# Kernel tuning notes

Measured on AMD Instinct MI355X. Metric: run time of the kernel, lower is better.

Reference implementation:

```python
import jax, jax.numpy as jnp
import numpy as np

B, V, M, H, L, T = 4, 2048, 8192, 64, 5, 4


def setup_inputs() -> dict:
    key = jax.random.key(0)
    ks = jax.random.split(key, 24)
    inp = {
        "input_llr": jax.random.normal(ks[0], (B, V), jnp.float32),
        "message_to_var_mapping": jax.random.randint(ks[1], (M,), 0, V, jnp.int32),
        "message_types": jax.random.randint(ks[2], (M,), 0, T, jnp.int32),
        "var_to_check_adjacency": jax.random.uniform(ks[3], (M, M), jnp.float32),
        "check_to_var_adjacency": jax.random.uniform(ks[4], (M, M), jnp.float32),
    }
    s = 0.05
    # input_embedding: Linear(1, H)
    inp["w_in"] = jax.random.normal(ks[5], (H,), jnp.float32) * s
    inp["b_in"] = jax.random.normal(ks[6], (H,), jnp.float32) * s
    # per-layer params, stacked over L iterations
    inp["type_emb"] = jax.random.normal(ks[7], (L, T, H), jnp.float32) * s
    inp["w1v"] = jax.random.normal(ks[8], (L, 2 * H, H), jnp.float32) * s
    inp["b1v"] = jax.random.normal(ks[9], (L, H), jnp.float32) * s
    inp["w2v"] = jax.random.normal(ks[10], (L, H, H), jnp.float32) * s
    inp["b2v"] = jax.random.normal(ks[11], (L, H), jnp.float32) * s
    inp["w1c"] = jax.random.normal(ks[12], (L, 2 * H, H), jnp.float32) * s
    inp["b1c"] = jax.random.normal(ks[13], (L, H), jnp.float32) * s
    inp["w2c"] = jax.random.normal(ks[14], (L, H, H), jnp.float32) * s
    inp["b2c"] = jax.random.normal(ks[15], (L, H), jnp.float32) * s
    # output_projection of the LAST gnn layer (the one used by decode_messages)
    inp["proj_w"] = jax.random.normal(ks[16], (H,), jnp.float32) * s
    inp["proj_b"] = jax.random.normal(ks[17], (), jnp.float32) * s
    return inp


def reference(input_llr, message_to_var_mapping, message_types,
              var_to_check_adjacency, check_to_var_adjacency,
              w_in, b_in, type_emb, w1v, b1v, w2v, b2v,
              w1c, b1c, w2c, b2c, proj_w, proj_b):
    Bv, Vn = input_llr.shape
    # gather message LLRs from variable nodes: (B, M)
    msg_llr = input_llr[:, message_to_var_mapping]
    # input embedding Linear(1, H): (B, M, H)
    feat = msg_llr[..., None] * w_in + b_in
    safe_types = jnp.clip(message_types, 0, T - 1)
    n_layers = type_emb.shape[0]
    for i in range(n_layers):
        te = type_emb[i][safe_types]                      # (M, H)
        comb = feat + te                                  # (B, M, H)
        v2c = jnp.einsum('mn,bnh->bmh', var_to_check_adjacency, comb)
        uv = jnp.concatenate([comb, v2c], axis=-1)        # (B, M, 2H)
        uv = jax.nn.relu(uv @ w1v[i] + b1v[i]) @ w2v[i] + b2v[i]
        c2v = jnp.einsum('mn,bnh->bmh', check_to_var_adjacency, comb)
        uc = jnp.concatenate([comb, c2v], axis=-1)
        uc = jax.nn.relu(uc @ w1c[i] + b1c[i]) @ w2c[i] + b2c[i]
        upd = uv + uc
        if i > 0:  # residual applied only after first iteration (per source)
            upd = upd + feat
        feat = upd
    # decode with last layer's output projection: (B, M)
    decoded = feat @ proj_w + proj_b
    # sum-aggregate message LLRs back to variable nodes: (B, V)
    var_llrs = jax.ops.segment_sum(decoded.T, message_to_var_mapping,
                                   num_segments=Vn).T
    return jax.nn.sigmoid(var_llrs + input_llr)
```

## Files before the change

kernel.cpp:

```cpp
#include <hip/hip_runtime.h>
#include <math.h>

static constexpr int CB = 4;
static constexpr int CV = 2048;
static constexpr int CM = 8192;
static constexpr int CH = 64;
static constexpr int CL = 5;
static constexpr int CT = 4;
static constexpr int RR = CM * CB;
static constexpr int WCAT_STRIDE = 192 * 128 + 128 * 64 + 128 + 64;

typedef float f32x4 __attribute__((ext_vector_type(4)));
typedef short bf16x8 __attribute__((ext_vector_type(8)));
typedef unsigned int u32;
typedef unsigned short u16;

__device__ inline u16 f2bf(float x) {
    u32 u = __float_as_uint(x);
    u += 0x7FFF + ((u >> 16) & 1);
    return (u16)(u >> 16);
}
__device__ inline float bf2f(u16 b) { return __uint_as_float(((u32)b) << 16); }

#define GLOAD16(gp, lp)                                                         \
    __builtin_amdgcn_global_load_lds(                                           \
        (const __attribute__((address_space(1))) unsigned int*)(gp),            \
        (__attribute__((address_space(3))) unsigned int*)(lp), 16, 0, 0)

__global__ void k_init_feat(const float* __restrict__ llr, const int* __restrict__ map,
                            const float* __restrict__ w_in, const float* __restrict__ b_in,
                            float* __restrict__ feat) {
    int idx = blockIdx.x * blockDim.x + threadIdx.x;
    int h = idx & 63;
    int r = idx >> 6;
    int m = r >> 2;
    int b = r & 3;
    float v = llr[b * CV + map[m]];
    feat[idx] = v * w_in[h] + b_in[h];
}

__global__ void k_comb(const float* __restrict__ feat, const int* __restrict__ types,
                       const float* __restrict__ te, float* __restrict__ in2) {
    int idx = blockIdx.x * blockDim.x + threadIdx.x;
    int h = idx & 63;
    int r = idx >> 6;
    int m = r >> 2;
    int t = types[m];
    t = t < 0 ? 0 : (t > CT - 1 ? CT - 1 : t);
    in2[(size_t)r * 192 + h] = feat[idx] + te[t * CH + h];
}

__global__ __launch_bounds__(256) void k_splitA(const float* __restrict__ Avc,
                                                const float* __restrict__ Acv,
                                                u16* __restrict__ Aprep) {
    __shared__ float lds[16][516];
    const int blk = blockIdx.x;
    const int adj = blk >> 13;
    const int rem = blk & 8191;
    const int rf = rem & 511;
    const int kig = rem >> 9;
    const float* __restrict__ A = adj ? Acv : Avc;
    const int t = threadIdx.x;
    {
        const int rl = t >> 4, cc = t & 15;
        const float* rp = A + (size_t)(rf * 16 + rl) * CM + kig * 512 + cc * 32;
#pragma unroll
        for (int j = 0; j < 8; ++j) {
            float4 v = *(const float4*)(rp + j * 4);
            *(float4*)&lds[rl][cc * 32 + j * 4] = v;
        }
    }
    __syncthreads();
    {
        const int r = t & 15, kl = t >> 4;
        float e[32];
#pragma unroll
        for (int j = 0; j < 8; ++j) {
            float4 v = *(const float4*)&lds[r][kl * 32 + j * 4];
            e[j * 4 + 0] = v.x; e[j * 4 + 1] = v.y;
            e[j * 4 + 2] = v.z; e[j * 4 + 3] = v.w;
        }
        const size_t base = (((size_t)adj * 256 + kig * 16 + kl) * 512 + rf) * 1024;
#pragma unroll
        for (int c = 0; c < 4; ++c) {
            u32 hw[4], lw[4];
#pragma unroll
            for (int j = 0; j < 4; ++j) {
                float a0 = e[c * 8 + 2 * j], a1 = e[c * 8 + 2 * j + 1];
                u16 h0 = f2bf(a0), h1 = f2bf(a1);
                u16 g0 = f2bf(a0 - bf2f(h0)), g1 = f2bf(a1 - bf2f(h1));
                hw[j] = (u32)h0 | ((u32)h1 << 16);
                lw[j] = (u32)g0 | ((u32)g1 << 16);
            }
            u16* dp = Aprep + base + (size_t)(r + 16 * c) * 8;
            *(uint4*)dp = make_uint4(hw[0], hw[1], hw[2], hw[3]);
            *(uint4*)(dp + 512) = make_uint4(lw[0], lw[1], lw[2], lw[3]);
        }
    }
}

__global__ void k_transposeB(const float* __restrict__ feat, const int* __restrict__ types,
                             const float* __restrict__ te, char* __restrict__ BprepC,
                             float* __restrict__ comb) {
    __shared__ float tile[64][65];
    __shared__ float teL[4][64];
    __shared__ int ty[64];
    const int tid = threadIdx.x;
    const int m0 = blockIdx.x * 64;
    teL[tid >> 6][tid & 63] = te[tid];
    if (tid < 64) {
        int tt = types[m0 + tid];
        ty[tid] = tt < 0 ? 0 : (tt > CT - 1 ? CT - 1 : tt);
    }
    __syncthreads();
    for (int b = 0; b < 4; ++b) {
        __syncthreads();
        {
            const int mr = tid >> 2, hc = (tid & 3) * 16;
            const float* fp = feat + ((size_t)(m0 + mr) * 4 + b) * 64 + hc;
            float* op = comb + ((size_t)(m0 + mr) * 4 + b) * 64 + hc;
            const int tt = ty[mr];
#pragma unroll
            for (int j = 0; j < 4; ++j) {
                float4 v = *(const float4*)(fp + j * 4);
                float4 c;
                c.x = v.x + teL[tt][hc + j * 4 + 0];
                c.y = v.y + teL[tt][hc + j * 4 + 1];
                c.z = v.z + teL[tt][hc + j * 4 + 2];
                c.w = v.w + teL[tt][hc + j * 4 + 3];
                tile[mr][hc + j * 4 + 0] = c.x;
                tile[mr][hc + j * 4 + 1] = c.y;
                tile[mr][hc + j * 4 + 2] = c.z;
                tile[mr][hc + j * 4 + 3] = c.w;
                *(float4*)(op + j * 4) = c;
            }
        }
        __syncthreads();
        {
            const int h = tid & 63, mg = tid >> 6;
            u32 hw[8], lw[8];
#pragma unroll
            for (int q = 0; q < 8; ++q) {
                float v0 = tile[mg * 16 + 2 * q + 0][h];
                float v1 = tile[mg * 16 + 2 * q + 1][h];
                u16 h0 = f2bf(v0), h1 = f2bf(v1);
                u16 g0 = f2bf(v0 - bf2f(h0)), g1 = f2bf(v1 - bf2f(h1));
                hw[q] = (u32)h0 | ((u32)h1 << 16);
                lw[q] = (u32)g0 | ((u32)g1 << 16);
            }
            const int c = b * 64 + h;
            const int mstart = m0 + mg * 16;
            const int ki = mstart >> 5;
            const int q0 = (mstart >> 3) & 3;
            const int swzc = (c & 7) << 4;
            char* rowp = BprepC + (size_t)ki * 32768 + c * 128;
            *(uint4*)(rowp + (((q0 + 0) * 16) ^ swzc)) = make_uint4(hw[0], hw[1], hw[2], hw[3]);
            *(uint4*)(rowp + (((q0 + 1) * 16) ^ swzc)) = make_uint4(hw[4], hw[5], hw[6], hw[7]);
            *(uint4*)(rowp + (((4 + q0) * 16) ^ swzc)) = make_uint4(lw[0], lw[1], lw[2], lw[3]);
            *(uint4*)(rowp + (((5 + q0) * 16) ^ swzc)) = make_uint4(lw[4], lw[5], lw[6], lw[7]);
        }
    }
}

__global__ __launch_bounds__(512, 1) void k_adjmfma_fast(
    const char* __restrict__ AprepC, const char* __restrict__ BprepC,
    float* __restrict__ pbuf) {
    __shared__ char frames[3][49152];

    int lin = blockIdx.y * 64 + blockIdx.x;
    lin = (lin & 7) * 32 + (lin >> 3);
    const int bx = lin & 63;
    const int by = lin >> 6;
    const int adj = by >> 1;
    const int ks = by & 1;

    const int tid = threadIdx.x;
    const int lane = tid & 63;
    const int wid = tid >> 6;
    const int wr = wid >> 2;
    const int wc = wid & 3;
    const int l15 = lane & 15, l4 = lane >> 4;
    const int m0 = bx * 128;

    const size_t abase = (((size_t)adj * 256) * 512 + (size_t)bx * 8) * 2048;

#define STAGE3(FP, S)                                                            \
    {                                                                            \
        int ki_ = ks * 128 + (S); if (ki_ > 255) ki_ = 255;                      \
        const char* as_ = AprepC + abase + (size_t)ki_ * (512 * 2048);           \
        GLOAD16(as_ + tid * 16, (FP) + tid * 16);                                \
        GLOAD16(as_ + 8192 + tid * 16, (FP) + 8192 + tid * 16);                  \
        const char* bs_ = BprepC + ((size_t)ki_ << 15);                          \
        GLOAD16(bs_ + tid * 16, (FP) + 16384 + tid * 16);                        \
        GLOAD16(bs_ + 8192 + tid * 16, (FP) + 24576 + tid * 16);                 \
        GLOAD16(bs_ + 16384 + tid * 16, (FP) + 32768 + tid * 16);                \
        GLOAD16(bs_ + 24576 + tid * 16, (FP) + 40960 + tid * 16);                \
    }

    f32x4 acc[4][4] = {};

    STAGE3(&frames[0][0], 0);
    STAGE3(&frames[1][0], 1);
    STAGE3(&frames[2][0], 2);

    int f = 0;
    for (int s = 0; s < 128; ++s) {
        asm volatile("s_waitcnt vmcnt(12)" ::: "memory");
        asm volatile("s_barrier" ::: "memory");
        const char* fr = &frames[f][0];
        bf16x8 bh[4], bl[4];
#pragma unroll
        for (int nf = 0; nf < 4; ++nf) {
            const int col = wc * 64 + nf * 16 + l15;
            const char* rb = fr + 16384 + col * 128;
            const int swz = (col & 7) << 4;
            bh[nf] = *(const bf16x8*)(rb + ((l4 * 16) ^ swz));
            bl[nf] = *(const bf16x8*)(rb + (((4 + l4) * 16) ^ swz));
        }
#pragma unroll
        for (int mf = 0; mf < 4; ++mf) {
            const char* ra = fr + (wr * 4 + mf) * 2048 + lane * 16;
            bf16x8 ah = *(const bf16x8*)ra;
            bf16x8 al = *(const bf16x8*)(ra + 1024);
#pragma unroll
            for (int nf = 0; nf < 4; ++nf) {
                acc[mf][nf] = __builtin_amdgcn_mfma_f32_16x16x32_bf16(ah, bh[nf], acc[mf][nf], 0, 0, 0);
                acc[mf][nf] = __builtin_amdgcn_mfma_f32_16x16x32_bf16(ah, bl[nf], acc[mf][nf], 0, 0, 0);
                acc[mf][nf] = __builtin_amdgcn_mfma_f32_16x16x32_bf16(al, bh[nf], acc[mf][nf], 0, 0, 0);
            }
        }
        asm volatile("s_barrier" ::: "memory");
        STAGE3(fr, s + 3);
        f = (f == 2) ? 0 : f + 1;
    }
    asm volatile("s_waitcnt vmcnt(0)" ::: "memory");

    float* pb = pbuf + (size_t)by * ((size_t)CM * 256);
#pragma unroll
    for (int mf = 0; mf < 4; ++mf) {
#pragma unroll
        for (int nf = 0; nf < 4; ++nf) {
            const int col = wc * 64 + nf * 16 + l15;
#pragma unroll
            for (int r = 0; r < 4; ++r) {
                const int m = m0 + wr * 64 + mf * 16 + l4 * 4 + r;
                pb[(size_t)m * 256 + col] = acc[mf][nf][r];
            }
        }
    }
#undef STAGE3
}

__global__ __launch_bounds__(256) void k_gemm1f(
    const float* __restrict__ comb, const float* __restrict__ pbuf,
    const float* __restrict__ wc, float* __restrict__ hid) {
    __shared__ float As[32][64];
    __shared__ float Bs[32][68];

    const int tid = threadIdx.x;
    const int m0 = blockIdx.y * 64;
    const int c0 = blockIdx.x * 64;
    const int tm = (tid & 15) * 4;
    const int tn = (tid >> 4) * 4;
    const int arow = tid & 63;
    const int akg = (tid >> 6) * 8;
    const int bk = tid >> 4;
    const int bc = (tid & 15) * 4;
    const float* bias = wc + 32768;

    float acc[4][4] = {};

    for (int k0 = 0; k0 < 192; k0 += 32) {
        const int krow = k0 + akg;
        const int r = m0 + arow;
        float4 a0, a1;
        if (krow < 64) {
            const float* ap = comb + (size_t)r * 64 + krow;
            a0 = *(const float4*)ap;
            a1 = *(const float4*)(ap + 4);
        } else {
            const int adj = (krow - 64) >> 6;
            const int h = (krow - 64) & 63;
            const float* p = pbuf + (size_t)(adj * 2) * ((size_t)CM * 256)
                           + (size_t)(r >> 2) * 256 + (r & 3) * 64 + h;
            float4 x0 = *(const float4*)p;
            float4 x1 = *(const float4*)(p + 4);
            float4 y0 = *(const float4*)(p + (size_t)CM * 256);
            float4 y1 = *(const float4*)(p + (size_t)CM * 256 + 4);
            a0.x = x0.x + y0.x; a0.y = x0.y + y0.y; a0.z = x0.z + y0.z; a0.w = x0.w + y0.w;
            a1.x = x1.x + y1.x; a1.y = x1.y + y1.y; a1.z = x1.z + y1.z; a1.w = x1.w + y1.w;
        }
        float4 b0 = *(const float4*)(wc + (size_t)(k0 + bk) * 128 + c0 + bc);
        float4 b1 = *(const float4*)(wc + (size_t)(k0 + bk + 16) * 128 + c0 + bc);
        As[akg + 0][arow] = a0.x;
        As[akg + 1][arow] = a0.y;
        As[akg + 2][arow] = a0.z;
        As[akg + 3][arow] = a0.w;
        As[akg + 4][arow] = a1.x;
        As[akg + 5][arow] = a1.y;
        As[akg + 6][arow] = a1.z;
        As[akg + 7][arow] = a1.w;
        *(float4*)&Bs[bk][bc] = b0;
        *(float4*)&Bs[bk + 16][bc] = b1;
        __syncthreads();
#pragma unroll
        for (int k = 0; k < 32; ++k) {
            float4 av = *(const float4*)&As[k][tm];
            float4 bv = *(const float4*)&Bs[k][tn];
            float a_[4] = {av.x, av.y, av.z, av.w};
            float b_[4] = {bv.x, bv.y, bv.z, bv.w};
#pragma unroll
            for (int i = 0; i < 4; ++i)
#pragma unroll
                for (int j = 0; j < 4; ++j)
                    acc[i][j] = fmaf(a_[i], b_[j], acc[i][j]);
        }
        __syncthreads();
    }

#pragma unroll
    for (int i = 0; i < 4; ++i) {
        int m = m0 + tm + i;
        float4 x = make_float4(acc[i][0], acc[i][1], acc[i][2], acc[i][3]);
        const float4 bv = *(const float4*)&bias[c0 + tn];
        x.x = fmaxf(x.x + bv.x, 0.f);
        x.y = fmaxf(x.y + bv.y, 0.f);
        x.z = fmaxf(x.z + bv.z, 0.f);
        x.w = fmaxf(x.w + bv.w, 0.f);
        *(float4*)&hid[(size_t)m * 128 + c0 + tn] = x;
    }
}

__global__ void k_transpose(const float* __restrict__ feat, const int* __restrict__ types,
                            const float* __restrict__ te,
                            u16* __restrict__ BH, u16* __restrict__ BL) {
    __shared__ float tile[64][65];
    __shared__ float teL[4][64];
    __shared__ int ty[64];
    const int tid = threadIdx.x;
    const int m0 = blockIdx.x * 64;
    teL[tid >> 6][tid & 63] = te[tid];
    if (tid < 64) {
        int t = types[m0 + tid];
        ty[tid] = t < 0 ? 0 : (t > CT - 1 ? CT - 1 : t);
    }
    __syncthreads();
    for (int b = 0; b < 4; ++b) {
        __syncthreads();
        {
            const int mr = tid >> 2, hc = (tid & 3) * 16;
            const float* fp = feat + ((size_t)(m0 + mr) * 4 + b) * 64 + hc;
            const int t = ty[mr];
#pragma unroll
            for (int j = 0; j < 4; ++j) {
                float4 v = *(const float4*)(fp + j * 4);
                tile[mr][hc + j * 4 + 0] = v.x + teL[t][hc + j * 4 + 0];
                tile[mr][hc + j * 4 + 1] = v.y + teL[t][hc + j * 4 + 1];
                tile[mr][hc + j * 4 + 2] = v.z + teL[t][hc + j * 4 + 2];
                tile[mr][hc + j * 4 + 3] = v.w + teL[t][hc + j * 4 + 3];
            }
        }
        __syncthreads();
        {
            const int h = tid & 63, mg = tid >> 6;
            u32 hw[8], lw[8];
#pragma unroll
            for (int q = 0; q < 8; ++q) {
                float v0 = tile[mg * 16 + 2 * q + 0][h];
                float v1 = tile[mg * 16 + 2 * q + 1][h];
                u16 h0 = f2bf(v0), h1 = f2bf(v1);
                u16 g0 = f2bf(v0 - bf2f(h0)), g1 = f2bf(v1 - bf2f(h1));
                hw[q] = (u32)h0 | ((u32)h1 << 16);
                lw[q] = (u32)g0 | ((u32)g1 << 16);
            }
            size_t obase = (size_t)(b * 64 + h) * CM + m0 + mg * 16;
            *(uint4*)(BH + obase) = make_uint4(hw[0], hw[1], hw[2], hw[3]);
            *(uint4*)(BH + obase + 8) = make_uint4(hw[4], hw[5], hw[6], hw[7]);
            *(uint4*)(BL + obase) = make_uint4(lw[0], lw[1], lw[2], lw[3]);
            *(uint4*)(BL + obase + 8) = make_uint4(lw[4], lw[5], lw[6], lw[7]);
        }
    }
}

__global__ __launch_bounds__(512, 2) void k_adjmfma_fb(
    const float* __restrict__ A0, const float* __restrict__ A1,
    const u16* __restrict__ BH, const u16* __restrict__ BL,
    float* __restrict__ pbuf) {
    __shared__ char lA[128 * 128];
    __shared__ char lB[256 * 128];

    const int tid = threadIdx.x;
    const int adj = blockIdx.y >> 1;
    const int ks = blockIdx.y & 1;
    const int m0 = blockIdx.x * 128;
    const float* __restrict__ A = adj ? A1 : A0;
    const int kbase = ks * 4096;

    const int lane = tid & 63;
    const int wid = tid >> 6;
    const int wr = wid >> 2;
    const int wc = wid & 3;
    const int l15 = lane & 15, l4 = lane >> 4;

    const int sa_row = tid >> 2, sa_kq = tid & 3;
    const int sb_col = tid >> 1, sb_part = tid & 1;

    f32x4 acc[4][4] = {};

    for (int k0 = 0; k0 < 4096; k0 += 32) {
        {
            const float* ap = A + (size_t)(m0 + sa_row) * CM + kbase + k0 + sa_kq * 8;
            float4 v0 = *(const float4*)ap;
            float4 v1 = *(const float4*)(ap + 4);
            float vv[8] = {v0.x, v0.y, v0.z, v0.w, v1.x, v1.y, v1.z, v1.w};
            u32 hw[4], lw[4];
#pragma unroll
            for (int j = 0; j < 4; ++j) {
                float a0 = vv[2 * j], a1 = vv[2 * j + 1];
                u16 h0 = f2bf(a0), h1 = f2bf(a1);
                u16 g0 = f2bf(a0 - bf2f(h0)), g1 = f2bf(a1 - bf2f(h1));
                hw[j] = (u32)h0 | ((u32)h1 << 16);
                lw[j] = (u32)g0 | ((u32)g1 << 16);
            }
            char* base = lA + sa_row * 128;
            const int swz = (sa_row & 7) << 4;
            *(uint4*)(base + ((sa_kq * 16) ^ swz)) = make_uint4(hw[0], hw[1], hw[2], hw[3]);
            *(uint4*)(base + ((64 + sa_kq * 16) ^ swz)) = make_uint4(lw[0], lw[1], lw[2], lw[3]);
        }
        {
            const u16* src = (sb_part ? BL : BH) + (size_t)sb_col * CM + kbase + k0;
            char* base = lB + sb_col * 128;
            const int swz = (sb_col & 7) << 4;
            const int lb = sb_part * 64;
#pragma unroll
            for (int j = 0; j < 4; ++j) {
                uint4 v = *(const uint4*)(src + j * 8);
                *(uint4*)(base + ((lb + j * 16) ^ swz)) = v;
            }
        }
        __syncthreads();

        bf16x8 bh[4], bl[4];
#pragma unroll
        for (int nf = 0; nf < 4; ++nf) {
            const int col = wc * 64 + nf * 16 + l15;
            const char* rb = lB + col * 128;
            const int swz = (col & 7) << 4;
            bh[nf] = *(const bf16x8*)(rb + ((l4 * 16) ^ swz));
            bl[nf] = *(const bf16x8*)(rb + ((64 + l4 * 16) ^ swz));
        }
#pragma unroll
        for (int mf = 0; mf < 4; ++mf) {
            const int row = wr * 64 + mf * 16 + l15;
            const char* ra = lA + row * 128;
            const int swz = (row & 7) << 4;
            bf16x8 ah = *(const bf16x8*)(ra + ((l4 * 16) ^ swz));
            bf16x8 al = *(const bf16x8*)(ra + ((64 + l4 * 16) ^ swz));
#pragma unroll
            for (int nf = 0; nf < 4; ++nf) {
                acc[mf][nf] = __builtin_amdgcn_mfma_f32_16x16x32_bf16(ah, bh[nf], acc[mf][nf], 0, 0, 0);
                acc[mf][nf] = __builtin_amdgcn_mfma_f32_16x16x32_bf16(ah, bl[nf], acc[mf][nf], 0, 0, 0);
                acc[mf][nf] = __builtin_amdgcn_mfma_f32_16x16x32_bf16(al, bh[nf], acc[mf][nf], 0, 0, 0);
            }
        }
        __syncthreads();
    }

    float* pb = pbuf + (size_t)blockIdx.y * ((size_t)CM * 256);
#pragma unroll
    for (int mf = 0; mf < 4; ++mf) {
#pragma unroll
        for (int nf = 0; nf < 4; ++nf) {
            const int col = wc * 64 + nf * 16 + l15;
#pragma unroll
            for (int r = 0; r < 4; ++r) {
                const int m = m0 + wr * 64 + mf * 16 + l4 * 4 + r;
                pb[(size_t)m * 256 + col] = acc[mf][nf][r];
            }
        }
    }
}

__global__ void k_reduce(const float* __restrict__ pbuf, float* __restrict__ in2) {
    int idx = blockIdx.x * blockDim.x + threadIdx.x;
    int adj = idx >> 19;
    int rem = idx & ((1 << 19) - 1);
    int m = rem >> 6;
    int f4 = rem & 63;
    size_t o = (size_t)m * 256 + (size_t)f4 * 4;
    const float* p0 = pbuf + (size_t)(adj * 2) * ((size_t)CM * 256);
    const float* p1 = p0 + (size_t)CM * 256;
    float4 a = *(const float4*)(p0 + o);
    float4 b4 = *(const float4*)(p1 + o);
    a.x += b4.x; a.y += b4.y; a.z += b4.z; a.w += b4.w;
    int col = f4 * 4;
    int bb = col >> 6, h = col & 63;
    *(float4*)&in2[((size_t)m * 4 + bb) * 192 + 64 + adj * 64 + h] = a;
}

__global__ void k_prep(const float* __restrict__ w1v, const float* __restrict__ b1v,
                       const float* __restrict__ w2v, const float* __restrict__ b2v,
                       const float* __restrict__ w1c, const float* __restrict__ b1c,
                       const float* __restrict__ w2c, const float* __restrict__ b2c,
                       float* __restrict__ wcat) {
    int idx = blockIdx.x * blockDim.x + threadIdx.x;
    int total = CL * WCAT_STRIDE;
    if (idx >= total) return;
    int i = idx / WCAT_STRIDE;
    int e = idx % WCAT_STRIDE;
    float v;
    if (e < 24576) {
        int j = e >> 7, k = e & 127;
        if (j < 64)        v = (k < 64) ? w1v[(i * 128 + j) * 64 + k]
                                        : w1c[(i * 128 + j) * 64 + (k - 64)];
        else if (j < 128)  v = (k < 64) ? w1v[(i * 128 + j) * 64 + k] : 0.f;
        else               v = (k < 64) ? 0.f : w1c[(i * 128 + (j - 64)) * 64 + (k - 64)];
    } else if (e < 32768) {
        int e2 = e - 24576; int k = e2 >> 6, h = e2 & 63;
        v = (k < 64) ? w2v[(i * 64 + k) * 64 + h]
                     : w2c[(i * 64 + (k - 64)) * 64 + h];
    } else if (e < 32896) {
        int k = e - 32768;
        v = (k < 64) ? b1v[i * 64 + k] : b1c[i * 64 + (k - 64)];
    } else {
        int h = e - 32896;
        v = b2v[i * 64 + h] + b2c[i * 64 + h];
    }
    wcat[idx] = v;
}

template<int OMODE, int RES>
__global__ __launch_bounds__(256) void k_gemm(
    const float* __restrict__ A0, int lda,
    const float* __restrict__ Bm, int ldb,
    float* __restrict__ O, const float* __restrict__ bias,
    const float* __restrict__ resid, int K) {
    __shared__ float As[32][64];
    __shared__ float Bs[32][68];

    const int tid = threadIdx.x;
    const int m0 = blockIdx.y * 64;
    const int c0 = blockIdx.x * 64;
    const int tm = (tid & 15) * 4;
    const int tn = (tid >> 4) * 4;
    const int arow = tid & 63;
    const int akg = (tid >> 6) * 8;
    const int bk = tid >> 4;
    const int bc = (tid & 15) * 4;

    float acc[4][4] = {};

    for (int k0 = 0; k0 < K; k0 += 32) {
        const float* Ap = A0 + (size_t)(m0 + arow) * (size_t)lda + k0 + akg;
        float4 a0 = *(const float4*)Ap;
        float4 a1 = *(const float4*)(Ap + 4);
        float4 b0 = *(const float4*)(Bm + (size_t)(k0 + bk) * (size_t)ldb + c0 + bc);
        float4 b1 = *(const float4*)(Bm + (size_t)(k0 + bk + 16) * (size_t)ldb + c0 + bc);
        As[akg + 0][arow] = a0.x;
        As[akg + 1][arow] = a0.y;
        As[akg + 2][arow] = a0.z;
        As[akg + 3][arow] = a0.w;
        As[akg + 4][arow] = a1.x;
        As[akg + 5][arow] = a1.y;
        As[akg + 6][arow] = a1.z;
        As[akg + 7][arow] = a1.w;
        *(float4*)&Bs[bk][bc] = b0;
        *(float4*)&Bs[bk + 16][bc] = b1;
        __syncthreads();
#pragma unroll
        for (int k = 0; k < 32; ++k) {
            float4 av = *(const float4*)&As[k][tm];
            float4 bv = *(const float4*)&Bs[k][tn];
            float a_[4] = {av.x, av.y, av.z, av.w};
            float b_[4] = {bv.x, bv.y, bv.z, bv.w};
#pragma unroll
            for (int i = 0; i < 4; ++i)
#pragma unroll
                for (int j = 0; j < 4; ++j)
                    acc[i][j] = fmaf(a_[i], b_[j], acc[i][j]);
        }
        __syncthreads();
    }

#pragma unroll
    for (int i = 0; i < 4; ++i) {
        int m = m0 + tm + i;
        float4 x = make_float4(acc[i][0], acc[i][1], acc[i][2], acc[i][3]);
        if (OMODE == 1) {
            const float4 bv = *(const float4*)&bias[c0 + tn];
            x.x = fmaxf(x.x + bv.x, 0.f);
            x.y = fmaxf(x.y + bv.y, 0.f);
            x.z = fmaxf(x.z + bv.z, 0.f);
            x.w = fmaxf(x.w + bv.w, 0.f);
            *(float4*)&O[(size_t)m * 128 + c0 + tn] = x;
        } else {
            const float4 bv = *(const float4*)&bias[tn];
            x.x += bv.x; x.y += bv.y; x.z += bv.z; x.w += bv.w;
            if (RES) {
                const float4 rv = *(const float4*)&resid[(size_t)m * 64 + tn];
                x.x += rv.x; x.y += rv.y; x.z += rv.z; x.w += rv.w;
            }
            *(float4*)&O[(size_t)m * 64 + tn] = x;
        }
    }
}

__global__ void k_zero(float* __restrict__ p, int n) {
    int i = blockIdx.x * blockDim.x + threadIdx.x;
    if (i < n) p[i] = 0.f;
}

__global__ void k_decode(const float* __restrict__ feat, const float* __restrict__ proj_w,
                         const float* __restrict__ proj_b, const int* __restrict__ map,
                         float* __restrict__ var_llrs) {
    int r = blockIdx.x * 4 + (threadIdx.x >> 6);
    int lane = threadIdx.x & 63;
    float v = feat[(size_t)r * 64 + lane] * proj_w[lane];
#pragma unroll
    for (int off = 32; off > 0; off >>= 1) v += __shfl_down(v, off);
    if (lane == 0) {
        int m = r >> 2, b = r & 3;
        atomicAdd(&var_llrs[b * CV + map[m]], v + proj_b[0]);
    }
}

__global__ void k_final(const float* __restrict__ var_llrs, const float* __restrict__ llr,
                        float* __restrict__ out) {
    int i = blockIdx.x * blockDim.x + threadIdx.x;
    float x = var_llrs[i] + llr[i];
    out[i] = 1.f / (1.f + expf(-x));
}

extern "C" void kernel_launch(void* const* d_in, const int* in_sizes, int n_in,
                              void* d_out, int out_size, void* d_ws, size_t ws_size,
                              hipStream_t stream) {
    const float* llr   = (const float*)d_in[0];
    const int*   map   = (const int*)d_in[1];
    const int*   types = (const int*)d_in[2];
    const float* Avc   = (const float*)d_in[3];
    const float* Acv   = (const float*)d_in[4];
    const float* w_in  = (const float*)d_in[5];
    const float* b_in  = (const float*)d_in[6];
    const float* temb  = (const float*)d_in[7];
    const float* w1v   = (const float*)d_in[8];
    const float* b1v   = (const float*)d_in[9];
    const float* w2v   = (const float*)d_in[10];
    const float* b2v   = (const float*)d_in[11];
    const float* w1c   = (const float*)d_in[12];
    const float* b1c   = (const float*)d_in[13];
    const float* w2c   = (const float*)d_in[14];
    const float* b2c   = (const float*)d_in[15];
    const float* projw = (const float*)d_in[16];
    const float* projb = (const float*)d_in[17];
    float* out = (float*)d_out;

    constexpr size_t OFF_FEAT = 0;
    constexpr size_t OFF_IN2  = OFF_FEAT + (size_t)RR * 64 * 4;
    constexpr size_t OFF_HID  = OFF_IN2 + (size_t)RR * 192 * 4;
    constexpr size_t OFF_WCAT = OFF_HID + (size_t)RR * 128 * 4;
    constexpr size_t OFF_VLLR = OFF_WCAT + (size_t)CL * WCAT_STRIDE * 4;
    constexpr size_t OFF_PBUF = OFF_VLLR + 8192 * 4;
    constexpr size_t OFF_X    = OFF_PBUF + (size_t)4 * CM * 256 * 4;
    constexpr size_t BPREP_BYTES = (size_t)256 * 256 * 128 + 32768;
    constexpr size_t OFF_APREP   = OFF_X + BPREP_BYTES;
    constexpr size_t APREP_BYTES = (size_t)2 * 256 * 512 * 2048 + 8192;
    constexpr size_t NEED_FAST   = OFF_APREP + APREP_BYTES;
    constexpr size_t OFF_CTH = OFF_X;
    constexpr size_t OFF_CTL = OFF_CTH + (size_t)256 * CM * 2;

    char* ws = (char*)d_ws;
    float* feat = (float*)(ws + OFF_FEAT);
    float* in2  = (float*)(ws + OFF_IN2);
    float* comb = (float*)(ws + OFF_IN2);
    float* hid  = (float*)(ws + OFF_HID);
    float* wcat = (float*)(ws + OFF_WCAT);
    float* vllr = (float*)(ws + OFF_VLLR);
    float* pbuf = (float*)(ws + OFF_PBUF);

    const bool fast = ws_size >= NEED_FAST;

    k_zero<<<(CB * CV + 255) / 256, 256, 0, stream>>>(vllr, CB * CV);
    k_prep<<<(CL * WCAT_STRIDE + 255) / 256, 256, 0, stream>>>(
        w1v, b1v, w2v, b2v, w1c, b1c, w2c, b2c, wcat);
    k_init_feat<<<(RR * CH) / 256, 256, 0, stream>>>(llr, map, w_in, b_in, feat);

    u16* Aprep = (u16*)(ws + OFF_APREP);
    char* Bprep = ws + OFF_X;
    u16* combTH = (u16*)(ws + OFF_CTH);
    u16* combTL = (u16*)(ws + OFF_CTL);

    if (fast)
        k_splitA<<<16384, 256, 0, stream>>>(Avc, Acv, Aprep);

    for (int i = 0; i < CL; ++i) {
        float* wc = wcat + (size_t)i * WCAT_STRIDE;
        const float* te = temb + i * CT * CH;
        if (fast) {
            k_transposeB<<<CM / 64, 256, 0, stream>>>(feat, types, te, Bprep, comb);
            k_adjmfma_fast<<<dim3(64, 4), 512, 0, stream>>>((const char*)Aprep, Bprep, pbuf);
            k_gemm1f<<<dim3(2, 512), 256, 0, stream>>>(comb, pbuf, wc, hid);
        } else {
            k_comb<<<(RR * CH) / 256, 256, 0, stream>>>(feat, types, te, in2);
            k_transpose<<<CM / 64, 256, 0, stream>>>(feat, types, te, combTH, combTL);
            k_adjmfma_fb<<<dim3(64, 4), 512, 0, stream>>>(Avc, Acv, combTH, combTL, pbuf);
            k_reduce<<<(2 * CM * 64) / 256, 256, 0, stream>>>(pbuf, in2);
            k_gemm<1, 0><<<dim3(2, 512), 256, 0, stream>>>(
                in2, 192, wc, 128, hid, wc + 32768, nullptr, 192);
        }
        if (i == 0)
            k_gemm<2, 0><<<dim3(1, 512), 256, 0, stream>>>(
                hid, 128, wc + 24576, 64, feat, wc + 32896, feat, 128);
        else
            k_gemm<2, 1><<<dim3(1, 512), 256, 0, stream>>>(
                hid, 128, wc + 24576, 64, feat, wc + 32896, feat, 128);
    }

    k_decode<<<RR / 4, 256, 0, stream>>>(feat, projw, projb, map, vllr);
    k_final<<<(CB * CV) / 256, 256, 0, stream>>>(vllr, llr, out);
}
```

Baseline: 1.352 ms.

## Split adjacency MFMA tiles over N halves, double-buffer LDS, pad splitA LDS

The adjacency GEMM kernel now splits the 256-wide output column dimension into two halves per block, doubling the grid to 512 blocks. Each block uses a smaller two-frame 32KB LDS double buffer instead of a three-frame 48KB triple buffer. Launch bounds now allow up to four blocks per CU, which raises occupancy and fills more CUs. The cost is that each A tile is loaded twice, once per column half, and the prefetch depth is shallower. The splitA transpose also gets a swizzled, padded LDS layout meant to cut bank conflicts.

```diff
diff --git a/kernel.cpp b/kernel.cpp
--- a/kernel.cpp
+++ b/kernel.cpp
@@ -9,6 +9,7 @@
 static constexpr int CT = 4;
 static constexpr int RR = CM * CB;
 static constexpr int WCAT_STRIDE = 192 * 128 + 128 * 64 + 128 + 64;
+static constexpr size_t SLAB = (size_t)CM * 256;
 
 typedef float f32x4 __attribute__((ext_vector_type(4)));
 typedef short bf16x8 __attribute__((ext_vector_type(8)));
@@ -53,7 +54,7 @@
 __global__ __launch_bounds__(256) void k_splitA(const float* __restrict__ Avc,
                                                 const float* __restrict__ Acv,
                                                 u16* __restrict__ Aprep) {
-    __shared__ float lds[16][516];
+    __shared__ float lds[16][548];
     const int blk = blockIdx.x;
     const int adj = blk >> 13;
     const int rem = blk & 8191;
@@ -64,19 +65,21 @@
     {
         const int rl = t >> 4, cc = t & 15;
         const float* rp = A + (size_t)(rf * 16 + rl) * CM + kig * 512 + cc * 32;
+        const int cbase = cc * 32 + ((cc & 7) << 2);
 #pragma unroll
         for (int j = 0; j < 8; ++j) {
             float4 v = *(const float4*)(rp + j * 4);
-            *(float4*)&lds[rl][cc * 32 + j * 4] = v;
+            *(float4*)&lds[rl][cbase + j * 4] = v;
         }
     }
     __syncthreads();
     {
         const int r = t & 15, kl = t >> 4;
+        const int cbase = kl * 32 + ((kl & 7) << 2);
         float e[32];
 #pragma unroll
         for (int j = 0; j < 8; ++j) {
-            float4 v = *(const float4*)&lds[r][kl * 32 + j * 4];
+            float4 v = *(const float4*)&lds[r][cbase + j * 4];
             e[j * 4 + 0] = v.x; e[j * 4 + 1] = v.y;
             e[j * 4 + 2] = v.z; e[j * 4 + 3] = v.w;
         }
@@ -162,17 +165,18 @@
     }
 }
 
-__global__ __launch_bounds__(512, 1) void k_adjmfma_fast(
+__global__ __launch_bounds__(512, 4) void k_adjmfma_fast(
     const char* __restrict__ AprepC, const char* __restrict__ BprepC,
     float* __restrict__ pbuf) {
-    __shared__ char frames[3][49152];
+    __shared__ char frames[2][32768];
 
     int lin = blockIdx.y * 64 + blockIdx.x;
-    lin = (lin & 7) * 32 + (lin >> 3);
-    const int bx = lin & 63;
-    const int by = lin >> 6;
-    const int adj = by >> 1;
-    const int ks = by & 1;
+    int g = (lin & 7) * 64 + (lin >> 3);
+    const int ns = g & 1;
+    const int bx = (g >> 1) & 63;
+    const int q  = g >> 7;
+    const int adj = q >> 1;
+    const int ks  = q & 1;
 
     const int tid = threadIdx.x;
     const int lane = tid & 63;
@@ -182,38 +186,36 @@
     const int l15 = lane & 15, l4 = lane >> 4;
     const int m0 = bx * 128;
 
-    const size_t abase = (((size_t)adj * 256) * 512 + (size_t)bx * 8) * 2048;
-
-#define STAGE3(FP, S)                                                            \
+    const size_t abase = (((size_t)adj * 256 + ks * 128) * 512 + (size_t)bx * 8) * 2048;
+    const size_t bbase = (((size_t)(ks * 128)) << 15) + (size_t)ns * 16384;
+
+#define STAGE(FR, S)                                                             \
     {                                                                            \
-        int ki_ = ks * 128 + (S); if (ki_ > 255) ki_ = 255;                      \
-        const char* as_ = AprepC + abase + (size_t)ki_ * (512 * 2048);           \
-        GLOAD16(as_ + tid * 16, (FP) + tid * 16);                                \
-        GLOAD16(as_ + 8192 + tid * 16, (FP) + 8192 + tid * 16);                  \
-        const char* bs_ = BprepC + ((size_t)ki_ << 15);                          \
-        GLOAD16(bs_ + tid * 16, (FP) + 16384 + tid * 16);                        \
-        GLOAD16(bs_ + 8192 + tid * 16, (FP) + 24576 + tid * 16);                 \
-        GLOAD16(bs_ + 16384 + tid * 16, (FP) + 32768 + tid * 16);                \
-        GLOAD16(bs_ + 24576 + tid * 16, (FP) + 40960 + tid * 16);                \
-    }
-
-    f32x4 acc[4][4] = {};
-
-    STAGE3(&frames[0][0], 0);
-    STAGE3(&frames[1][0], 1);
-    STAGE3(&frames[2][0], 2);
+        int s_ = (S) > 127 ? 127 : (S);                                          \
+        const char* as_ = AprepC + abase + (size_t)s_ * (512 * 2048);            \
+        GLOAD16(as_ + tid * 16, (FR) + tid * 16);                                \
+        GLOAD16(as_ + 8192 + tid * 16, (FR) + 8192 + tid * 16);                  \
+        const char* bs_ = BprepC + bbase + ((size_t)s_ << 15);                   \
+        GLOAD16(bs_ + tid * 16, (FR) + 16384 + tid * 16);                        \
+        GLOAD16(bs_ + 8192 + tid * 16, (FR) + 24576 + tid * 16);                 \
+    }
+
+    f32x4 acc[4][2] = {};
+
+    STAGE(&frames[0][0], 0);
 
     int f = 0;
     for (int s = 0; s < 128; ++s) {
-        asm volatile("s_waitcnt vmcnt(12)" ::: "memory");
+        STAGE(&frames[f ^ 1][0], s + 1);
+        asm volatile("s_waitcnt vmcnt(4)" ::: "memory");
         asm volatile("s_barrier" ::: "memory");
         const char* fr = &frames[f][0];
-        bf16x8 bh[4], bl[4];
-#pragma unroll
-        for (int nf = 0; nf < 4; ++nf) {
-            const int col = wc * 64 + nf * 16 + l15;
-            const char* rb = fr + 16384 + col * 128;
-            const int swz = (col & 7) << 4;
+        bf16x8 bh[2], bl[2];
+#pragma unroll
+        for (int nf = 0; nf < 2; ++nf) {
+            const int lc = wc * 32 + nf * 16 + l15;
+            const char* rb = fr + 16384 + lc * 128;
+            const int swz = (lc & 7) << 4;
             bh[nf] = *(const bf16x8*)(rb + ((l4 * 16) ^ swz));
             bl[nf] = *(const bf16x8*)(rb + (((4 + l4) * 16) ^ swz));
         }
@@ -223,24 +225,23 @@
             bf16x8 ah = *(const bf16x8*)ra;
             bf16x8 al = *(const bf16x8*)(ra + 1024);
 #pragma unroll
-            for (int nf = 0; nf < 4; ++nf) {
+            for (int nf = 0; nf < 2; ++nf) {
                 acc[mf][nf] = __builtin_amdgcn_mfma_f32_16x16x32_bf16(ah, bh[nf], acc[mf][nf], 0, 0, 0);
                 acc[mf][nf] = __builtin_amdgcn_mfma_f32_16x16x32_bf16(ah, bl[nf], acc[mf][nf], 0, 0, 0);
                 acc[mf][nf] = __builtin_amdgcn_mfma_f32_16x16x32_bf16(al, bh[nf], acc[mf][nf], 0, 0, 0);
             }
         }
         asm volatile("s_barrier" ::: "memory");
-        STAGE3(fr, s + 3);
-        f = (f == 2) ? 0 : f + 1;
+        f ^= 1;
     }
     asm volatile("s_waitcnt vmcnt(0)" ::: "memory");
 
-    float* pb = pbuf + (size_t)by * ((size_t)CM * 256);
+    float* pb = pbuf + (size_t)q * SLAB;
 #pragma unroll
     for (int mf = 0; mf < 4; ++mf) {
 #pragma unroll
-        for (int nf = 0; nf < 4; ++nf) {
-            const int col = wc * 64 + nf * 16 + l15;
+        for (int nf = 0; nf < 2; ++nf) {
+            const int col = ns * 128 + wc * 32 + nf * 16 + l15;
 #pragma unroll
             for (int r = 0; r < 4; ++r) {
                 const int m = m0 + wr * 64 + mf * 16 + l4 * 4 + r;
@@ -248,7 +249,7 @@
             }
         }
     }
-#undef STAGE3
+#undef STAGE
 }
 
 __global__ __launch_bounds__(256) void k_gemm1f(
@@ -281,12 +282,12 @@
         } else {
             const int adj = (krow - 64) >> 6;
             const int h = (krow - 64) & 63;
-            const float* p = pbuf + (size_t)(adj * 2) * ((size_t)CM * 256)
+            const float* p = pbuf + (size_t)(adj * 2) * SLAB
                            + (size_t)(r >> 2) * 256 + (r & 3) * 64 + h;
             float4 x0 = *(const float4*)p;
             float4 x1 = *(const float4*)(p + 4);
-            float4 y0 = *(const float4*)(p + (size_t)CM * 256);
-            float4 y1 = *(const float4*)(p + (size_t)CM * 256 + 4);
+            float4 y0 = *(const float4*)(p + SLAB);
+            float4 y1 = *(const float4*)(p + SLAB + 4);
             a0.x = x0.x + y0.x; a0.y = x0.y + y0.y; a0.z = x0.z + y0.z; a0.w = x0.w + y0.w;
             a1.x = x1.x + y1.x; a1.y = x1.y + y1.y; a1.z = x1.z + y1.z; a1.w = x1.w + y1.w;
         }
@@ -466,7 +467,7 @@
         __syncthreads();
     }
 
-    float* pb = pbuf + (size_t)blockIdx.y * ((size_t)CM * 256);
+    float* pb = pbuf + (size_t)blockIdx.y * SLAB;
 #pragma unroll
     for (int mf = 0; mf < 4; ++mf) {
 #pragma unroll
@@ -488,8 +489,8 @@
     int m = rem >> 6;
     int f4 = rem & 63;
     size_t o = (size_t)m * 256 + (size_t)f4 * 4;
-    const float* p0 = pbuf + (size_t)(adj * 2) * ((size_t)CM * 256);
-    const float* p1 = p0 + (size_t)CM * 256;
+    const float* p0 = pbuf + (size_t)(adj * 2) * SLAB;
+    const float* p1 = p0 + SLAB;
     float4 a = *(const float4*)(p0 + o);
     float4 b4 = *(const float4*)(p1 + o);
     a.x += b4.x; a.y += b4.y; a.z += b4.z; a.w += b4.w;
@@ -660,8 +661,8 @@
     constexpr size_t OFF_WCAT = OFF_HID + (size_t)RR * 128 * 4;
     constexpr size_t OFF_VLLR = OFF_WCAT + (size_t)CL * WCAT_STRIDE * 4;
     constexpr size_t OFF_PBUF = OFF_VLLR + 8192 * 4;
-    constexpr size_t OFF_X    = OFF_PBUF + (size_t)4 * CM * 256 * 4;
-    constexpr size_t BPREP_BYTES = (size_t)256 * 256 * 128 + 32768;
+    constexpr size_t OFF_X    = OFF_PBUF + (size_t)4 * SLAB * 4;
+    constexpr size_t BPREP_BYTES = (size_t)256 * 32768 + 32768;
     constexpr size_t OFF_APREP   = OFF_X + BPREP_BYTES;
     constexpr size_t APREP_BYTES = (size_t)2 * 256 * 512 * 2048 + 8192;
     constexpr size_t NEED_FAST   = OFF_APREP + APREP_BYTES;
@@ -676,6 +677,10 @@
     float* wcat = (float*)(ws + OFF_WCAT);
     float* vllr = (float*)(ws + OFF_VLLR);
     float* pbuf = (float*)(ws + OFF_PBUF);
+    char* Bprep = ws + OFF_X;
+    u16* combTH = (u16*)(ws + OFF_CTH);
+    u16* combTL = (u16*)(ws + OFF_CTL);
+    u16* Aprep  = (u16*)(ws + OFF_APREP);
 
     const bool fast = ws_size >= NEED_FAST;
 
@@ -683,11 +688,6 @@
     k_prep<<<(CL * WCAT_STRIDE + 255) / 256, 256, 0, stream>>>(
         w1v, b1v, w2v, b2v, w1c, b1c, w2c, b2c, wcat);
     k_init_feat<<<(RR * CH) / 256, 256, 0, stream>>>(llr, map, w_in, b_in, feat);
-
-    u16* Aprep = (u16*)(ws + OFF_APREP);
-    char* Bprep = ws + OFF_X;
-    u16* combTH = (u16*)(ws + OFF_CTH);
-    u16* combTL = (u16*)(ws + OFF_CTL);
 
     if (fast)
         k_splitA<<<16384, 256, 0, stream>>>(Avc, Acv, Aprep);
@@ -697,7 +697,8 @@
         const float* te = temb + i * CT * CH;
         if (fast) {
             k_transposeB<<<CM / 64, 256, 0, stream>>>(feat, types, te, Bprep, comb);
-            k_adjmfma_fast<<<dim3(64, 4), 512, 0, stream>>>((const char*)Aprep, Bprep, pbuf);
+            k_adjmfma_fast<<<dim3(64, 8), 512, 0, stream>>>(
+                (const char*)Aprep, Bprep, pbuf);
             k_gemm1f<<<dim3(2, 512), 256, 0, stream>>>(comb, pbuf, wc, hid);
         } else {
             k_comb<<<(RR * CH) / 256, 256, 0, stream>>>(feat, types, te, in2);
```

After: 1.399 ms. +3.5%, slower.
